# Kernel tuning notes

Measured on AMD Instinct MI355X. Metric: run time of the kernel, lower is better.

Reference implementation:

```python
import jax, jax.numpy as jnp
import numpy as np
import math

B, N, DIM, H, D = 2, 2048, 1024, 16, 64
EXPECTED_K = 1.0
LAYERSCALE_INIT = 0.001
EPS = 1e-6  # flax LayerNorm default


def layer_norm(x, scale, bias):
    mu = jnp.mean(x, axis=-1, keepdims=True)
    var = jnp.mean((x - mu) ** 2, axis=-1, keepdims=True)
    return (x - mu) * jax.lax.rsqrt(var + EPS) * scale + bias


def setup_inputs() -> dict:
    key = jax.random.key(0)
    ks = jax.random.split(key, 8)
    s = DIM ** -0.5
    x = jax.random.normal(ks[0], (B, N, DIM), jnp.float32)
    Wq = jax.random.normal(ks[1], (DIM, H * D), jnp.float32) * s
    Wk = jax.random.normal(ks[2], (DIM, H * D), jnp.float32) * s
    Wv = jax.random.normal(ks[3], (DIM, H * D), jnp.float32) * s
    Wo = jax.random.normal(ks[4], (H * D, DIM), jnp.float32) * ((H * D) ** -0.5)
    e = EXPECTED_K / N
    init_bias = jnp.full((1, 1, 1, 1), math.log(e / (1.0 - e)), jnp.float32)
    return {
        'x': x,
        'Wq': Wq, 'bq': jnp.zeros((H * D,), jnp.float32),
        'Wk': Wk, 'bk': jnp.zeros((H * D,), jnp.float32),
        'Wv': Wv, 'bv': jnp.zeros((H * D,), jnp.float32),
        'qn_scale': jnp.ones((D,), jnp.float32), 'qn_bias': jnp.zeros((D,), jnp.float32),
        'kn_scale': jnp.ones((D,), jnp.float32), 'kn_bias': jnp.zeros((D,), jnp.float32),
        'init_bias': init_bias,
        'Wo': Wo, 'bo': jnp.zeros((DIM,), jnp.float32),
        'gamma': jnp.full((DIM,), LAYERSCALE_INIT, jnp.float32),
    }


def reference(x, Wq, bq, Wk, bk, Wv, bv, qn_scale, qn_bias, kn_scale, kn_bias,
              init_bias, Wo, bo, gamma):
    Bv, Nv, _ = x.shape
    q = (x @ Wq + bq).reshape(Bv, Nv, H, D)
    k = (x @ Wk + bk).reshape(Bv, Nv, H, D)
    v = (x @ Wv + bv).reshape(Bv, Nv, H, D)
    q = layer_norm(q, qn_scale, qn_bias)
    k = layer_norm(k, kn_scale, kn_bias)
    q = jnp.swapaxes(q, 1, 2)  # [B,H,N,D]
    k = jnp.swapaxes(k, 1, 2)
    v = jnp.swapaxes(v, 1, 2)
    # NOTE: original code computes scale = head_dim**-0.5 but never applies it.
    attn_logits = jnp.einsum('bhid,bhjd->bhij', q, k)
    attn_weights = jax.nn.sigmoid(attn_logits + init_bias)
    out = jnp.einsum('bhij,bhjd->bhid', attn_weights, v)
    out = jnp.swapaxes(out, 1, 2).reshape(Bv, Nv, H * D)
    out = out @ Wo + bo
    return out * gamma
```

## Files before the change

### kernel.cpp

```cpp
#include <hip/hip_runtime.h>

#define DEV static __device__ __forceinline__

typedef __bf16 bf16x8 __attribute__((ext_vector_type(8)));
typedef __bf16 bf16x4 __attribute__((ext_vector_type(4)));
typedef float f32x4 __attribute__((ext_vector_type(4)));
typedef float f32x16 __attribute__((ext_vector_type(16)));
typedef unsigned int uint4v __attribute__((ext_vector_type(4)));
typedef unsigned short ushort4v __attribute__((ext_vector_type(4)));
using u16 = unsigned short;

#define NN 2048
#define DIMD 1024

DEV u16 f2bf(float f) {
    __bf16 b = (__bf16)f;
    return __builtin_bit_cast(u16, b);
}
DEV float bf2f(u16 s) {
    unsigned u = ((unsigned)s) << 16;
    return __builtin_bit_cast(float, u);
}
DEV bf16x8 load16(const u16* p) { return __builtin_bit_cast(bf16x8, *(const uint4v*)p); }
DEV f32x4 mfma16(bf16x8 a, bf16x8 b, f32x4 c) {
    return __builtin_amdgcn_mfma_f32_16x16x32_bf16(a, b, c, 0, 0, 0);
}
DEV f32x16 mfma32(bf16x8 a, bf16x8 b, f32x16 c) {
    return __builtin_amdgcn_mfma_f32_32x32x16_bf16(a, b, c, 0, 0, 0);
}
DEV void gl_lds16(const u16* g, u16* l) {
    __builtin_amdgcn_global_load_lds((const __attribute__((address_space(1))) void*)g,
                                     (__attribute__((address_space(3))) void*)l, 16, 0, 0);
}


__global__ __launch_bounds__(256) void k_pack_x(const float* __restrict__ x,
                                                u16* __restrict__ xb, int n4) {
    int i = blockIdx.x * 256 + threadIdx.x;
    if (i >= n4) return;
    float4 v = ((const float4*)x)[i];
    ushort4v o;
    o[0] = f2bf(v.x); o[1] = f2bf(v.y); o[2] = f2bf(v.z); o[3] = f2bf(v.w);
    *(ushort4v*)(xb + (size_t)i * 4) = o;
}

__global__ __launch_bounds__(256) void k_transpose_w(const float* __restrict__ s0,
                                                     const float* __restrict__ s1,
                                                     const float* __restrict__ s2,
                                                     const float* __restrict__ s3,
                                                     u16* __restrict__ wqkv_t,
                                                     u16* __restrict__ wo_t) {
    __shared__ float tile[32][33];
    int z = blockIdx.z;
    const float* src = (z == 0) ? s0 : (z == 1) ? s1 : (z == 2) ? s2 : s3;
    u16* dst = (z < 3) ? (wqkv_t + (size_t)z * 1024 * 1024) : wo_t;
    int tx = threadIdx.x & 31, ty = threadIdx.x >> 5;
    int kb = blockIdx.y * 32, nb = blockIdx.x * 32;
#pragma unroll
    for (int j = 0; j < 4; ++j)
        tile[ty + 8 * j][tx] = src[(size_t)(kb + ty + 8 * j) * 1024 + nb + tx];
    __syncthreads();
#pragma unroll
    for (int j = 0; j < 4; ++j)
        dst[(size_t)(nb + ty + 8 * j) * 1024 + kb + tx] = f2bf(tile[tx][ty + 8 * j]);
}

__global__ __launch_bounds__(256) void k_gemm_qkv(const u16* __restrict__ A,
                                                  const u16* __restrict__ Bt,
                                                  const float* __restrict__ bq,
                                                  const float* __restrict__ bk,
                                                  const float* __restrict__ bv,
                                                  const float* __restrict__ qs,
                                                  const float* __restrict__ qb,
                                                  const float* __restrict__ ks,
                                                  const float* __restrict__ kb_,
                                                  u16* __restrict__ Qf,
                                                  u16* __restrict__ Kf,
                                                  u16* __restrict__ Vf) {
    __shared__ u16 As[128 * 32];
    __shared__ u16 Bs[128 * 32];
    const int K = 1024;
    const int m0 = blockIdx.x * 128, n0 = blockIdx.y * 128;
    const int tid = threadIdx.x;
    const int lane = tid & 63, w = tid >> 6;
    const int wr = w >> 1, wc = w & 1;
    const int li = lane & 15, g = lane >> 4;

    f32x4 acc[4][4] = {};

    const u16* gA = A + (size_t)(m0 + w * 16 + (lane >> 2)) * K + (lane & 3) * 8;
    const u16* gB = Bt + (size_t)(n0 + w * 16 + (lane >> 2)) * K + (lane & 3) * 8;
    u16* lA = &As[(w * 16) * 32];
    u16* lB = &Bs[(w * 16) * 32];

    for (int k0 = 0; k0 < K; k0 += 32) {
        __syncthreads();
        gl_lds16(gA + k0, lA);
        gl_lds16(gA + (size_t)64 * K + k0, lA + 64 * 32);
        gl_lds16(gB + k0, lB);
        gl_lds16(gB + (size_t)64 * K + k0, lB + 64 * 32);
        asm volatile("s_waitcnt vmcnt(0)" ::: "memory");
        __syncthreads();
        bf16x8 af[4], bfv[4];
#pragma unroll
        for (int mi = 0; mi < 4; ++mi)
            af[mi] = load16(&As[(wr * 64 + mi * 16 + li) * 32 + g * 8]);
#pragma unroll
        for (int ni = 0; ni < 4; ++ni)
            bfv[ni] = load16(&Bs[(wc * 64 + ni * 16 + li) * 32 + g * 8]);
#pragma unroll
        for (int mi = 0; mi < 4; ++mi)
#pragma unroll
            for (int ni = 0; ni < 4; ++ni)
                acc[mi][ni] = mfma16(af[mi], bfv[ni], acc[mi][ni]);
    }

    const int col0 = n0 + wc * 64;
    const int seg = col0 >> 10;
    const int hcol = col0 & 1023;
    const int h = hcol >> 6;

    if (seg < 2) {
        const float* S = (seg == 0) ? qs : ks;
        const float* Bb = (seg == 0) ? qb : kb_;
        const float* bias = (seg == 0) ? bq : bk;
        u16* dst = (seg == 0) ? Qf : Kf;
        float lnS[4], lnB[4], bv4[4];
#pragma unroll
        for (int ni = 0; ni < 4; ++ni) {
            int d = ni * 16 + li;
            lnS[ni] = S[d]; lnB[ni] = Bb[d]; bv4[ni] = bias[hcol + d];
        }
#pragma unroll
        for (int mi = 0; mi < 4; ++mi) {
#pragma unroll
            for (int r = 0; r < 4; ++r) {
                float v0 = acc[mi][0][r] + bv4[0];
                float v1 = acc[mi][1][r] + bv4[1];
                float v2 = acc[mi][2][r] + bv4[2];
                float v3 = acc[mi][3][r] + bv4[3];
                float s1 = v0 + v1 + v2 + v3;
                float s2 = v0 * v0 + v1 * v1 + v2 * v2 + v3 * v3;
#pragma unroll
                for (int o = 1; o < 16; o <<= 1) {
                    s1 += __shfl_xor(s1, o);
                    s2 += __shfl_xor(s2, o);
                }
                float mu = s1 * (1.0f / 64.0f);
                float var = s2 * (1.0f / 64.0f) - mu * mu;
                float rsv = rsqrtf(var + 1e-6f);
                int row = m0 + wr * 64 + mi * 16 + 4 * g + r;
                int bseq = row >> 11, n = row & 2047;
                size_t base = ((size_t)(bseq * 16 + h)) * 131072 +
                              ((size_t)(n >> 5) * 4) * 512 + (size_t)(n & 31) * 8 +
                              (li >> 3) * 256 + (li & 7);
                dst[base + 0 * 512] = f2bf((v0 - mu) * rsv * lnS[0] + lnB[0]);
                dst[base + 1 * 512] = f2bf((v1 - mu) * rsv * lnS[1] + lnB[1]);
                dst[base + 2 * 512] = f2bf((v2 - mu) * rsv * lnS[2] + lnB[2]);
                dst[base + 3 * 512] = f2bf((v3 - mu) * rsv * lnS[3] + lnB[3]);
            }
        }
    } else {
        float bv4[4];
#pragma unroll
        for (int ni = 0; ni < 4; ++ni) bv4[ni] = bv[hcol + ni * 16 + li];
#pragma unroll
        for (int mi = 0; mi < 4; ++mi) {
#pragma unroll
            for (int r = 0; r < 4; ++r) {
                int row = m0 + wr * 64 + mi * 16 + 4 * g + r;
                int bseq = row >> 11, j = row & 2047;
                size_t vb_ = ((size_t)(bseq * 16 + h)) * 131072 +
                             ((size_t)((j >> 5) * 4 + ((j >> 4) & 1))) * 512 +
                             (size_t)(((j >> 3) & 1) * 32) * 8 + (j & 7);
#pragma unroll
                for (int ni = 0; ni < 4; ++ni)
                    Vf[vb_ + (ni >> 1) * 1024 + ((ni & 1) * 16 + li) * 8] =
                        f2bf(acc[mi][ni][r] + bv4[ni]);
            }
        }
    }
}

__global__ __launch_bounds__(256) void k_gemm_out(const u16* __restrict__ A,
                                                  const u16* __restrict__ Bt,
                                                  const float* __restrict__ bias,
                                                  const float* __restrict__ gamma,
                                                  float* __restrict__ out) {
    __shared__ u16 As[128 * 32];
    __shared__ u16 Bs[128 * 32];
    const int K = 1024, ldc = 1024;
    const int m0 = blockIdx.x * 128, n0 = blockIdx.y * 128;
    const int tid = threadIdx.x;
    const int lane = tid & 63, w = tid >> 6;
    const int wr = w >> 1, wc = w & 1;
    const int li = lane & 15, g = lane >> 4;

    f32x4 acc[4][4] = {};

    const u16* gA = A + (size_t)(m0 + w * 16 + (lane >> 2)) * K + (lane & 3) * 8;
    const u16* gB = Bt + (size_t)(n0 + w * 16 + (lane >> 2)) * K + (lane & 3) * 8;
    u16* lA = &As[(w * 16) * 32];
    u16* lB = &Bs[(w * 16) * 32];

    for (int k0 = 0; k0 < K; k0 += 32) {
        __syncthreads();
        gl_lds16(gA + k0, lA);
        gl_lds16(gA + (size_t)64 * K + k0, lA + 64 * 32);
        gl_lds16(gB + k0, lB);
        gl_lds16(gB + (size_t)64 * K + k0, lB + 64 * 32);
        asm volatile("s_waitcnt vmcnt(0)" ::: "memory");
        __syncthreads();
        bf16x8 af[4], bfv[4];
#pragma unroll
        for (int mi = 0; mi < 4; ++mi)
            af[mi] = load16(&As[(wr * 64 + mi * 16 + li) * 32 + g * 8]);
#pragma unroll
        for (int ni = 0; ni < 4; ++ni)
            bfv[ni] = load16(&Bs[(wc * 64 + ni * 16 + li) * 32 + g * 8]);
#pragma unroll
        for (int mi = 0; mi < 4; ++mi)
#pragma unroll
            for (int ni = 0; ni < 4; ++ni)
                acc[mi][ni] = mfma16(af[mi], bfv[ni], acc[mi][ni]);
    }

#pragma unroll
    for (int mi = 0; mi < 4; ++mi) {
        int row = m0 + wr * 64 + mi * 16 + 4 * g;
#pragma unroll
        for (int ni = 0; ni < 4; ++ni) {
            int col = n0 + wc * 64 + ni * 16 + li;
            float bv_ = bias[col], gv = gamma[col];
            f32x4 v = acc[mi][ni];
#pragma unroll
            for (int r = 0; r < 4; ++r)
                out[(size_t)(row + r) * ldc + col] = (v[r] + bv_) * gv;
        }
    }
}

__global__ __launch_bounds__(256) void k_attn(const u16* __restrict__ Qf,
                                              const u16* __restrict__ Kf,
                                              const u16* __restrict__ Vf,
                                              const float* __restrict__ ib,
                                              u16* __restrict__ attn_out) {
    __shared__ float red[2][64][65];
    const int bid = blockIdx.x;
    const int xcd = bid & 7, idx = bid >> 3;
    const int bh = xcd * 4 + (idx >> 5);
    const int iblk = idx & 31;
    const int b = bh >> 4, h = bh & 15;
    const int tid = threadIdx.x;
    const int jq = tid >> 6, lane = tid & 63;
    const int l32 = lane & 31, hi = lane >> 5;
    const float c0 = -ib[0] * 1.44269504f;
    const float c1 = -1.44269504f;
    const u16* Qb = Qf + (size_t)bh * 131072;
    const u16* Kb = Kf + (size_t)bh * 131072;
    const u16* Vb = Vf + (size_t)bh * 131072;
    const int it0 = iblk * 2;

    bf16x8 qf[2][4];
#pragma unroll
    for (int t = 0; t < 2; ++t)
#pragma unroll
        for (int s = 0; s < 4; ++s)
            qf[t][s] = load16(Qb + ((size_t)((it0 + t) * 4 + s)) * 512 + lane * 8);

    f32x16 accO[2][2] = {};
    const u16* kb0 = Kb + (size_t)(jq * 16) * 2048;
    const u16* vb0 = Vb + (size_t)(jq * 16) * 2048;

    bf16x8 kf[2][4];
#pragma unroll
    for (int s = 0; s < 4; ++s) kf[0][s] = load16(kb0 + s * 512 + lane * 8);

#pragma unroll
    for (int jt = 0; jt < 16; ++jt) {
        const int cur = jt & 1, nxt = cur ^ 1;
        if (jt < 15) {
            const u16* kbn = kb0 + (size_t)(jt + 1) * 2048;
#pragma unroll
            for (int s = 0; s < 4; ++s) kf[nxt][s] = load16(kbn + s * 512 + lane * 8);
        }
        bf16x8 vf[2][2];
        const u16* vbc = vb0 + (size_t)jt * 2048;
#pragma unroll
        for (int db = 0; db < 2; ++db)
#pragma unroll
            for (int js = 0; js < 2; ++js)
                vf[db][js] = load16(vbc + (db * 2 + js) * 512 + lane * 8);
        __builtin_amdgcn_s_setprio(1);
        f32x16 sa[2] = {f32x16{}, f32x16{}};
#pragma unroll
        for (int s = 0; s < 4; ++s) sa[0] = mfma32(kf[cur][s], qf[0][s], sa[0]);
#pragma unroll
        for (int s = 0; s < 4; ++s) sa[1] = mfma32(kf[cur][s], qf[1][s], sa[1]);
        __builtin_amdgcn_s_setprio(0);
        bf16x8 pb[2][2];
#pragma unroll
        for (int t = 0; t < 2; ++t) {
            float p[16];
#pragma unroll
            for (int r = 0; r < 16; ++r) {
                float e = __builtin_amdgcn_exp2f(fmaf(sa[t][r], c1, c0));
                p[r] = __builtin_amdgcn_rcpf(1.0f + e);
            }
            unsigned wd[8];
#pragma unroll
            for (int u = 0; u < 8; ++u) {
                unsigned r_;
                asm("v_cvt_pk_bf16_f32 %0, %1, %2"
                    : "=v"(r_) : "v"(p[2 * u]), "v"(p[2 * u + 1]));
                wd[u] = r_;
            }
            asm("v_permlane32_swap_b32 %0, %1" : "+v"(wd[0]), "+v"(wd[2]));
            asm("v_permlane32_swap_b32 %0, %1" : "+v"(wd[1]), "+v"(wd[3]));
            asm("v_permlane32_swap_b32 %0, %1" : "+v"(wd[4]), "+v"(wd[6]));
            asm("v_permlane32_swap_b32 %0, %1" : "+v"(wd[5]), "+v"(wd[7]));
            uint4v u0 = {wd[0], wd[1], wd[2], wd[3]};
            uint4v u1 = {wd[4], wd[5], wd[6], wd[7]};
            pb[t][0] = __builtin_bit_cast(bf16x8, u0);
            pb[t][1] = __builtin_bit_cast(bf16x8, u1);
        }
        __builtin_amdgcn_s_setprio(1);
#pragma unroll
        for (int t = 0; t < 2; ++t)
#pragma unroll
            for (int db = 0; db < 2; ++db)
#pragma unroll
                for (int js = 0; js < 2; ++js)
                    accO[t][db] = mfma32(vf[db][js], pb[t][js], accO[t][db]);
        __builtin_amdgcn_s_setprio(0);
    }

    if (jq & 1) {
#pragma unroll
        for (int t = 0; t < 2; ++t)
#pragma unroll
            for (int db = 0; db < 2; ++db)
#pragma unroll
                for (int r = 0; r < 16; ++r)
                    red[jq >> 1][t * 32 + l32][db * 32 + (r & 3) + 8 * (r >> 2) + 4 * hi] =
                        accO[t][db][r];
    }
    __syncthreads();
    if (!(jq & 1)) {
#pragma unroll
        for (int t = 0; t < 2; ++t)
#pragma unroll
            for (int db = 0; db < 2; ++db)
#pragma unroll
                for (int r = 0; r < 16; ++r)
                    accO[t][db][r] +=
                        red[jq >> 1][t * 32 + l32][db * 32 + (r & 3) + 8 * (r >> 2) + 4 * hi];
    }
    __syncthreads();
    if (jq == 2) {
#pragma unroll
        for (int t = 0; t < 2; ++t)
#pragma unroll
            for (int db = 0; db < 2; ++db)
#pragma unroll
                for (int r = 0; r < 16; ++r)
                    red[0][t * 32 + l32][db * 32 + (r & 3) + 8 * (r >> 2) + 4 * hi] =
                        accO[t][db][r];
    }
    __syncthreads();
    if (jq == 0) {
#pragma unroll
        for (int t = 0; t < 2; ++t)
#pragma unroll
            for (int db = 0; db < 2; ++db)
#pragma unroll
                for (int r = 0; r < 16; ++r)
                    accO[t][db][r] +=
                        red[0][t * 32 + l32][db * 32 + (r & 3) + 8 * (r >> 2) + 4 * hi];
#pragma unroll
        for (int t = 0; t < 2; ++t) {
            const int i = it0 * 32 + t * 32 + l32;
#pragma unroll
            for (int db = 0; db < 2; ++db)
#pragma unroll
                for (int q = 0; q < 4; ++q) {
                    int d = db * 32 + 8 * q + 4 * hi;
                    bf16x4 o4;
#pragma unroll
                    for (int r = 0; r < 4; ++r) o4[r] = (__bf16)accO[t][db][4 * q + r];
                    *(bf16x4*)&attn_out[(size_t)(b * NN + i) * 1024 + h * 64 + d] = o4;
                }
        }
    }
}


extern "C" void kernel_launch(void* const* d_in, const int* in_sizes, int n_in,
                              void* d_out, int out_size, void* d_ws, size_t ws_size,
                              hipStream_t stream) {
    (void)in_sizes; (void)n_in; (void)out_size; (void)ws_size;
    const float* x     = (const float*)d_in[0];
    const float* Wq    = (const float*)d_in[1];
    const float* bq    = (const float*)d_in[2];
    const float* Wk    = (const float*)d_in[3];
    const float* bk    = (const float*)d_in[4];
    const float* Wv    = (const float*)d_in[5];
    const float* bv    = (const float*)d_in[6];
    const float* qn_s  = (const float*)d_in[7];
    const float* qn_b  = (const float*)d_in[8];
    const float* kn_s  = (const float*)d_in[9];
    const float* kn_b  = (const float*)d_in[10];
    const float* ib    = (const float*)d_in[11];
    const float* Wo    = (const float*)d_in[12];
    const float* bo    = (const float*)d_in[13];
    const float* gamma = (const float*)d_in[14];
    float* out = (float*)d_out;

    char* ws = (char*)d_ws;
    size_t off = 0;
    auto alloc = [&](size_t bytes) -> void* {
        void* p = ws + off;
        off += (bytes + 255) & ~(size_t)255;
        return p;
    };
    u16* xb       = (u16*)alloc((size_t)4096 * 1024 * 2);
    u16* wqkv_t   = (u16*)alloc((size_t)3072 * 1024 * 2);
    u16* wo_t     = (u16*)alloc((size_t)1024 * 1024 * 2);
    u16* Qf       = (u16*)alloc((size_t)32 * 131072 * 2);
    u16* Kf       = (u16*)alloc((size_t)32 * 131072 * 2);
    u16* Vf       = (u16*)alloc((size_t)32 * 131072 * 2);
    u16* attn_out = (u16*)alloc((size_t)4096 * 1024 * 2);

    k_pack_x<<<4096, 256, 0, stream>>>(x, xb, 1048576);
    k_transpose_w<<<dim3(32, 32, 4), 256, 0, stream>>>(Wq, Wk, Wv, Wo, wqkv_t, wo_t);
    k_gemm_qkv<<<dim3(32, 24), 256, 0, stream>>>(xb, wqkv_t, bq, bk, bv,
                                                 qn_s, qn_b, kn_s, kn_b, Qf, Kf, Vf);
    k_attn<<<1024, 256, 0, stream>>>(Qf, Kf, Vf, ib, attn_out);
    k_gemm_out<<<dim3(32, 8), 256, 0, stream>>>(attn_out, wo_t, bo, gamma, out);
}
```

Baseline: 131.4 us.

## Software-pipeline QK and PV MFMAs in attention, merge prep kernels

The attention inner loop is restructured so the QK^T MFMAs for the next tile's first query block run while the sigmoid and pack of the current scores execute. K fragments are now prefetched two tiles ahead, and sched_barriers pin the interleaving. The kernel also gets launch_bounds(256,2) to target two blocks per CU. Separately, the x bf16 pack and weight transpose kernels are merged into one launch to save a launch. Risks are higher register pressure under the occupancy bound and possible spills.

Result: faster. 126.5 us (-3.7%).

```diff
diff --git a/kernel.cpp b/kernel.cpp
--- a/kernel.cpp
+++ b/kernel.cpp
@@ -34,35 +34,39 @@
 }
 
 
-__global__ __launch_bounds__(256) void k_pack_x(const float* __restrict__ x,
-                                                u16* __restrict__ xb, int n4) {
-    int i = blockIdx.x * 256 + threadIdx.x;
-    if (i >= n4) return;
-    float4 v = ((const float4*)x)[i];
-    ushort4v o;
-    o[0] = f2bf(v.x); o[1] = f2bf(v.y); o[2] = f2bf(v.z); o[3] = f2bf(v.w);
-    *(ushort4v*)(xb + (size_t)i * 4) = o;
-}
-
-__global__ __launch_bounds__(256) void k_transpose_w(const float* __restrict__ s0,
-                                                     const float* __restrict__ s1,
-                                                     const float* __restrict__ s2,
-                                                     const float* __restrict__ s3,
-                                                     u16* __restrict__ wqkv_t,
-                                                     u16* __restrict__ wo_t) {
+__global__ __launch_bounds__(256) void k_prep(const float* __restrict__ x,
+                                              const float* __restrict__ s0,
+                                              const float* __restrict__ s1,
+                                              const float* __restrict__ s2,
+                                              const float* __restrict__ s3,
+                                              u16* __restrict__ xb,
+                                              u16* __restrict__ wqkv_t,
+                                              u16* __restrict__ wo_t) {
     __shared__ float tile[32][33];
-    int z = blockIdx.z;
-    const float* src = (z == 0) ? s0 : (z == 1) ? s1 : (z == 2) ? s2 : s3;
-    u16* dst = (z < 3) ? (wqkv_t + (size_t)z * 1024 * 1024) : wo_t;
-    int tx = threadIdx.x & 31, ty = threadIdx.x >> 5;
-    int kb = blockIdx.y * 32, nb = blockIdx.x * 32;
-#pragma unroll
-    for (int j = 0; j < 4; ++j)
-        tile[ty + 8 * j][tx] = src[(size_t)(kb + ty + 8 * j) * 1024 + nb + tx];
-    __syncthreads();
-#pragma unroll
-    for (int j = 0; j < 4; ++j)
-        dst[(size_t)(nb + ty + 8 * j) * 1024 + kb + tx] = f2bf(tile[tx][ty + 8 * j]);
+    const int z = blockIdx.z;
+    if (z < 4) {
+        const float* src = (z == 0) ? s0 : (z == 1) ? s1 : (z == 2) ? s2 : s3;
+        u16* dst = (z < 3) ? (wqkv_t + (size_t)z * 1024 * 1024) : wo_t;
+        int tx = threadIdx.x & 31, ty = threadIdx.x >> 5;
+        int kb = blockIdx.y * 32, nb = blockIdx.x * 32;
+#pragma unroll
+        for (int j = 0; j < 4; ++j)
+            tile[ty + 8 * j][tx] = src[(size_t)(kb + ty + 8 * j) * 1024 + nb + tx];
+        __syncthreads();
+#pragma unroll
+        for (int j = 0; j < 4; ++j)
+            dst[(size_t)(nb + ty + 8 * j) * 1024 + kb + tx] = f2bf(tile[tx][ty + 8 * j]);
+    } else {
+        const int bidx = blockIdx.y * 32 + blockIdx.x;
+#pragma unroll
+        for (int q = 0; q < 4; ++q) {
+            int i = bidx * 1024 + q * 256 + threadIdx.x;
+            float4 v = ((const float4*)x)[i];
+            ushort4v o;
+            o[0] = f2bf(v.x); o[1] = f2bf(v.y); o[2] = f2bf(v.z); o[3] = f2bf(v.w);
+            *(ushort4v*)(xb + (size_t)i * 4) = o;
+        }
+    }
 }
 
 __global__ __launch_bounds__(256) void k_gemm_qkv(const u16* __restrict__ A,
@@ -240,11 +244,11 @@
     }
 }
 
-__global__ __launch_bounds__(256) void k_attn(const u16* __restrict__ Qf,
-                                              const u16* __restrict__ Kf,
-                                              const u16* __restrict__ Vf,
-                                              const float* __restrict__ ib,
-                                              u16* __restrict__ attn_out) {
+__global__ __launch_bounds__(256, 2) void k_attn(const u16* __restrict__ Qf,
+                                                 const u16* __restrict__ Kf,
+                                                 const u16* __restrict__ Vf,
+                                                 const float* __restrict__ ib,
+                                                 u16* __restrict__ attn_out) {
     __shared__ float red[2][64][65];
     const int bid = blockIdx.x;
     const int xcd = bid & 7, idx = bid >> 3;
@@ -275,15 +279,15 @@
     bf16x8 kf[2][4];
 #pragma unroll
     for (int s = 0; s < 4; ++s) kf[0][s] = load16(kb0 + s * 512 + lane * 8);
+#pragma unroll
+    for (int s = 0; s < 4; ++s) kf[1][s] = load16(kb0 + 2048 + s * 512 + lane * 8);
+    f32x16 sa0 = {}, sa1;
+#pragma unroll
+    for (int s = 0; s < 4; ++s) sa0 = mfma32(kf[0][s], qf[0][s], sa0);
 
 #pragma unroll
     for (int jt = 0; jt < 16; ++jt) {
         const int cur = jt & 1, nxt = cur ^ 1;
-        if (jt < 15) {
-            const u16* kbn = kb0 + (size_t)(jt + 1) * 2048;
-#pragma unroll
-            for (int s = 0; s < 4; ++s) kf[nxt][s] = load16(kbn + s * 512 + lane * 8);
-        }
         bf16x8 vf[2][2];
         const u16* vbc = vb0 + (size_t)jt * 2048;
 #pragma unroll
@@ -292,28 +296,31 @@
             for (int js = 0; js < 2; ++js)
                 vf[db][js] = load16(vbc + (db * 2 + js) * 512 + lane * 8);
         __builtin_amdgcn_s_setprio(1);
-        f32x16 sa[2] = {f32x16{}, f32x16{}};
-#pragma unroll
-        for (int s = 0; s < 4; ++s) sa[0] = mfma32(kf[cur][s], qf[0][s], sa[0]);
-#pragma unroll
-        for (int s = 0; s < 4; ++s) sa[1] = mfma32(kf[cur][s], qf[1][s], sa[1]);
+        sa1 = f32x16{};
+#pragma unroll
+        for (int s = 0; s < 4; ++s) sa1 = mfma32(kf[cur][s], qf[1][s], sa1);
         __builtin_amdgcn_s_setprio(0);
-        bf16x8 pb[2][2];
-#pragma unroll
-        for (int t = 0; t < 2; ++t) {
+        if (jt < 14) {
+            const u16* kbn = kb0 + (size_t)(jt + 2) * 2048;
+#pragma unroll
+            for (int s = 0; s < 4; ++s) kf[cur][s] = load16(kbn + s * 512 + lane * 8);
+        }
+        __builtin_amdgcn_sched_barrier(0);
+        bf16x8 p00, p01;
+        {
             float p[16];
 #pragma unroll
             for (int r = 0; r < 16; ++r) {
-                float e = __builtin_amdgcn_exp2f(fmaf(sa[t][r], c1, c0));
+                float e = __builtin_amdgcn_exp2f(fmaf(sa0[r], c1, c0));
                 p[r] = __builtin_amdgcn_rcpf(1.0f + e);
             }
             unsigned wd[8];
 #pragma unroll
-            for (int u = 0; u < 8; ++u) {
+            for (int u2 = 0; u2 < 8; ++u2) {
                 unsigned r_;
                 asm("v_cvt_pk_bf16_f32 %0, %1, %2"
-                    : "=v"(r_) : "v"(p[2 * u]), "v"(p[2 * u + 1]));
-                wd[u] = r_;
+                    : "=v"(r_) : "v"(p[2 * u2]), "v"(p[2 * u2 + 1]));
+                wd[u2] = r_;
             }
             asm("v_permlane32_swap_b32 %0, %1" : "+v"(wd[0]), "+v"(wd[2]));
             asm("v_permlane32_swap_b32 %0, %1" : "+v"(wd[1]), "+v"(wd[3]));
@@ -321,17 +328,53 @@
             asm("v_permlane32_swap_b32 %0, %1" : "+v"(wd[5]), "+v"(wd[7]));
             uint4v u0 = {wd[0], wd[1], wd[2], wd[3]};
             uint4v u1 = {wd[4], wd[5], wd[6], wd[7]};
-            pb[t][0] = __builtin_bit_cast(bf16x8, u0);
-            pb[t][1] = __builtin_bit_cast(bf16x8, u1);
-        }
+            p00 = __builtin_bit_cast(bf16x8, u0);
+            p01 = __builtin_bit_cast(bf16x8, u1);
+        }
+        __builtin_amdgcn_sched_barrier(0);
         __builtin_amdgcn_s_setprio(1);
-#pragma unroll
-        for (int t = 0; t < 2; ++t)
-#pragma unroll
-            for (int db = 0; db < 2; ++db)
-#pragma unroll
-                for (int js = 0; js < 2; ++js)
-                    accO[t][db] = mfma32(vf[db][js], pb[t][js], accO[t][db]);
+        accO[0][0] = mfma32(vf[0][0], p00, accO[0][0]);
+        accO[0][0] = mfma32(vf[0][1], p01, accO[0][0]);
+        accO[0][1] = mfma32(vf[1][0], p00, accO[0][1]);
+        accO[0][1] = mfma32(vf[1][1], p01, accO[0][1]);
+        if (jt < 15) {
+            sa0 = f32x16{};
+#pragma unroll
+            for (int s = 0; s < 4; ++s) sa0 = mfma32(kf[nxt][s], qf[0][s], sa0);
+        }
+        __builtin_amdgcn_s_setprio(0);
+        __builtin_amdgcn_sched_barrier(0);
+        bf16x8 p10, p11;
+        {
+            float p[16];
+#pragma unroll
+            for (int r = 0; r < 16; ++r) {
+                float e = __builtin_amdgcn_exp2f(fmaf(sa1[r], c1, c0));
+                p[r] = __builtin_amdgcn_rcpf(1.0f + e);
+            }
+            unsigned wd[8];
+#pragma unroll
+            for (int u2 = 0; u2 < 8; ++u2) {
+                unsigned r_;
+                asm("v_cvt_pk_bf16_f32 %0, %1, %2"
+                    : "=v"(r_) : "v"(p[2 * u2]), "v"(p[2 * u2 + 1]));
+                wd[u2] = r_;
+            }
+            asm("v_permlane32_swap_b32 %0, %1" : "+v"(wd[0]), "+v"(wd[2]));
+            asm("v_permlane32_swap_b32 %0, %1" : "+v"(wd[1]), "+v"(wd[3]));
+            asm("v_permlane32_swap_b32 %0, %1" : "+v"(wd[4]), "+v"(wd[6]));
+            asm("v_permlane32_swap_b32 %0, %1" : "+v"(wd[5]), "+v"(wd[7]));
+            uint4v u0 = {wd[0], wd[1], wd[2], wd[3]};
+            uint4v u1 = {wd[4], wd[5], wd[6], wd[7]};
+            p10 = __builtin_bit_cast(bf16x8, u0);
+            p11 = __builtin_bit_cast(bf16x8, u1);
+        }
+        __builtin_amdgcn_sched_barrier(0);
+        __builtin_amdgcn_s_setprio(1);
+        accO[1][0] = mfma32(vf[0][0], p10, accO[1][0]);
+        accO[1][0] = mfma32(vf[0][1], p11, accO[1][0]);
+        accO[1][1] = mfma32(vf[1][0], p10, accO[1][1]);
+        accO[1][1] = mfma32(vf[1][1], p11, accO[1][1]);
         __builtin_amdgcn_s_setprio(0);
     }
 
@@ -431,8 +474,7 @@
     u16* Vf       = (u16*)alloc((size_t)32 * 131072 * 2);
     u16* attn_out = (u16*)alloc((size_t)4096 * 1024 * 2);
 
-    k_pack_x<<<4096, 256, 0, stream>>>(x, xb, 1048576);
-    k_transpose_w<<<dim3(32, 32, 4), 256, 0, stream>>>(Wq, Wk, Wv, Wo, wqkv_t, wo_t);
+    k_prep<<<dim3(32, 32, 5), 256, 0, stream>>>(x, Wq, Wk, Wv, Wo, xb, wqkv_t, wo_t);
     k_gemm_qkv<<<dim3(32, 24), 256, 0, stream>>>(xb, wqkv_t, bq, bk, bv,
                                                  qn_s, qn_b, kn_s, kn_b, Qf, Kf, Vf);
     k_attn<<<1024, 256, 0, stream>>>(Qf, Kf, Vf, ib, attn_out);
```
